# Performance work log

Measured on AMD Instinct MI355X. Metric: run time of the kernel, lower is better.

Reference implementation:

```python
import jax, jax.numpy as jnp
import numpy as np

NUM_HEADS = 16
HEAD_DIM = 128
HIDDEN = NUM_HEADS * HEAD_DIM


def rotate_half(x):
    x1, x2 = jnp.split(x, 2, axis=-1)
    return jnp.concatenate((-x2, x1), axis=-1)


def setup_inputs() -> dict:
    key = jax.random.key(0)
    ks = jax.random.split(key, 7)
    b, s = 2, 2048
    return {
        "hidden_states": jax.random.normal(ks[0], (b, s, HIDDEN), dtype=jnp.float32),
        "cos": jax.random.normal(ks[1], (1, 1, s, HEAD_DIM), dtype=jnp.float32),
        "sin": jax.random.normal(ks[2], (1, 1, s, HEAD_DIM), dtype=jnp.float32),
        "Wq": jax.random.normal(ks[3], (HIDDEN, HIDDEN), dtype=jnp.float32) * 0.02,
        "Wk": jax.random.normal(ks[4], (HIDDEN, HIDDEN), dtype=jnp.float32) * 0.02,
        "Wv": jax.random.normal(ks[5], (HIDDEN, HIDDEN), dtype=jnp.float32) * 0.02,
        "Wo": jax.random.normal(ks[6], (HIDDEN, HIDDEN), dtype=jnp.float32) * 0.02,
    }


def reference(hidden_states, cos, sin, Wq, Wk, Wv, Wo):
    b, s, _ = hidden_states.shape

    def proj(W):
        # [b,s,hidden] -> [b,H,s,D]
        return (hidden_states @ W).reshape(b, s, NUM_HEADS, HEAD_DIM).transpose(0, 2, 1, 3)

    q = proj(Wq)
    k = proj(Wk)
    v = proj(Wv)

    # RoPE: cos/sin [1,1,s,D] broadcast over batch and heads
    q = q * cos + rotate_half(q) * sin
    k = k * cos + rotate_half(k) * sin

    scale = 1.0 / jnp.sqrt(jnp.asarray(HEAD_DIM, dtype=q.dtype))
    scores = jnp.einsum("bhqd,bhkd->bhqk", q, k) * scale  # [b,H,s,s]
    attn = jax.nn.softmax(scores, axis=-1)  # no mask applied (matches source)
    out = jnp.einsum("bhqk,bhkd->bhqd", attn, v)  # [b,H,s,D]
    out = out.transpose(0, 2, 1, 3).reshape(b, s, HIDDEN)
    return out @ Wo
```

## Files before the change

kernel.cpp:

```cpp
#include <hip/hip_runtime.h>

typedef short bf16x8 __attribute__((ext_vector_type(8)));
typedef float f32x4 __attribute__((ext_vector_type(4)));

#define HID   2048
#define S_LEN 2048
#define NH    16
#define HD    128
#define BATCH 2
#define NROWS (BATCH * S_LEN)

__device__ __forceinline__ float bf2f(unsigned short u) {
    union { unsigned int i; float f; } v;
    v.i = ((unsigned int)u) << 16;
    return v.f;
}
__device__ __forceinline__ unsigned short f2bf(float f) {
    union { float f; unsigned int i; } v;
    v.f = f;
    unsigned int u = v.i;
    return (unsigned short)((u + 0x7fffu + ((u >> 16) & 1u)) >> 16);
}

__device__ __forceinline__ void async16(const unsigned short* g, unsigned short* l) {
    __builtin_amdgcn_global_load_lds(
        (const __attribute__((address_space(1))) unsigned int*)g,
        (__attribute__((address_space(3))) unsigned int*)l, 16, 0, 0);
}

__global__ __launch_bounds__(256) void cast_f32_bf16(const float* __restrict__ x,
                                                     unsigned short* __restrict__ y, int n) {
    int i = (blockIdx.x * 256 + threadIdx.x) * 4;
    if (i < n) {
        float4 v = *(const float4*)(x + i);
        ushort4 o;
        o.x = f2bf(v.x); o.y = f2bf(v.y); o.z = f2bf(v.z); o.w = f2bf(v.w);
        *(ushort4*)(y + i) = o;
    }
}

__global__ __launch_bounds__(256) void transpose_cast(const float* __restrict__ W,
                                                      unsigned short* __restrict__ WT) {
    __shared__ float tile[32][33];
    int tx = threadIdx.x, ty = threadIdx.y;
    int bx = blockIdx.x, by = blockIdx.y;
#pragma unroll
    for (int i = 0; i < 4; i++)
        tile[ty + i * 8][tx] = W[(size_t)(by * 32 + ty + i * 8) * HID + bx * 32 + tx];
    __syncthreads();
#pragma unroll
    for (int i = 0; i < 4; i++)
        WT[(size_t)(bx * 32 + ty + i * 8) * HID + by * 32 + tx] = f2bf(tile[tx][ty + i * 8]);
}

template <int MODE>
__global__ __launch_bounds__(256, 2) void gemm_bt(const unsigned short* __restrict__ A,
                                                  const unsigned short* __restrict__ Bt,
                                                  void* __restrict__ Cout) {
    __shared__ unsigned short Asm[128 * 32];
    __shared__ unsigned short Bsm[128 * 32];
    int t = threadIdx.x;
    int wave = t >> 6, lane = t & 63;
    int wm = wave >> 1, wn = wave & 1;
    int c = lane & 15, quad = lane >> 4;
    int m0 = blockIdx.y * 128, n0 = blockIdx.x * 128;

    int srow = wave * 32 + (lane >> 2);
    int scol = (lane & 3) * 8;
    const unsigned short* Ag = A + (size_t)(m0 + srow) * HID + scol;
    const unsigned short* Bg = Bt + (size_t)(n0 + srow) * HID + scol;
    unsigned short* Al = Asm + wave * 1024;
    unsigned short* Bl = Bsm + wave * 1024;

    f32x4 zero = {0.f, 0.f, 0.f, 0.f};
    f32x4 acc[4][4];
#pragma unroll
    for (int i = 0; i < 4; i++)
#pragma unroll
        for (int j = 0; j < 4; j++) acc[i][j] = zero;

    for (int k0 = 0; k0 < HID; k0 += 32) {
        async16(Ag + k0, Al);
        async16(Ag + k0 + 16 * HID, Al + 512);
        async16(Bg + k0, Bl);
        async16(Bg + k0 + 16 * HID, Bl + 512);
        __syncthreads();
        bf16x8 af[4], bfr[4];
#pragma unroll
        for (int mt = 0; mt < 4; mt++)
            af[mt] = *(const bf16x8*)(Asm + (wm * 64 + mt * 16 + c) * 32 + quad * 8);
#pragma unroll
        for (int nt = 0; nt < 4; nt++)
            bfr[nt] = *(const bf16x8*)(Bsm + (wn * 64 + nt * 16 + c) * 32 + quad * 8);
#pragma unroll
        for (int mt = 0; mt < 4; mt++)
#pragma unroll
            for (int nt = 0; nt < 4; nt++)
                acc[mt][nt] = __builtin_amdgcn_mfma_f32_16x16x32_bf16(af[mt], bfr[nt],
                                                                      acc[mt][nt], 0, 0, 0);
        __syncthreads();
    }

#pragma unroll
    for (int mt = 0; mt < 4; mt++) {
#pragma unroll
        for (int nt = 0; nt < 4; nt++) {
#pragma unroll
            for (int r = 0; r < 4; r++) {
                int row = m0 + wm * 64 + mt * 16 + quad * 4 + r;
                int col = n0 + wn * 64 + nt * 16 + c;
                float v = acc[mt][nt][r];
                if (MODE == 2) {
                    ((float*)Cout)[(size_t)row * HID + col] = v;
                } else {
                    int b = row >> 11, s = row & 2047;
                    int h = col >> 7, d = col & 127;
                    size_t idx;
                    if (MODE == 0) idx = ((size_t)(b * NH + h) * S_LEN + s) * HD + d;
                    else           idx = ((size_t)(b * NH + h) * HD + d) * S_LEN + s;
                    ((unsigned short*)Cout)[idx] = f2bf(v);
                }
            }
        }
    }
}

__global__ __launch_bounds__(256) void rope_kernel(unsigned short* __restrict__ Qb,
                                                   unsigned short* __restrict__ Kb,
                                                   const float* __restrict__ cosp,
                                                   const float* __restrict__ sinp) {
    unsigned short* P = blockIdx.y ? Kb : Qb;
    float scq = blockIdx.y ? 1.0f : 0.08838834764831845f;
    int idx = blockIdx.x * 256 + threadIdx.x;
    int row = idx >> 6, j = idx & 63;
    int s = row & (S_LEN - 1);
    size_t base = (size_t)row * HD;
    float x1 = bf2f(P[base + j]);
    float x2 = bf2f(P[base + j + 64]);
    float c1 = cosp[s * HD + j], s1 = sinp[s * HD + j];
    float c2 = cosp[s * HD + j + 64], s2 = sinp[s * HD + j + 64];
    P[base + j]      = f2bf((x1 * c1 - x2 * s1) * scq);
    P[base + j + 64] = f2bf((x2 * c2 + x1 * s2) * scq);
}

#define PKS 72
__global__ __launch_bounds__(256, 2) void attn_kernel(const unsigned short* __restrict__ Q,
                                                      const unsigned short* __restrict__ Kg,
                                                      const unsigned short* __restrict__ Vt,
                                                      unsigned short* __restrict__ Aout) {
    __shared__ unsigned short Ksm[64 * 128];
    __shared__ unsigned short Vsm[128 * 64];
    __shared__ __align__(16) unsigned short Psm[4 * 2 * 16 * PKS];
    int bh = blockIdx.y;
    int b = bh >> 4, h = bh & 15;
    int t = threadIdx.x;
    int wave = t >> 6, lane = t & 63;
    int c = lane & 15, quad = lane >> 4;
    int q0 = blockIdx.x * 128 + wave * 32;
    const unsigned short* Qp = Q + (size_t)bh * S_LEN * HD;
    const unsigned short* Kp = Kg + (size_t)bh * S_LEN * HD;
    const unsigned short* Vp = Vt + (size_t)bh * HD * S_LEN;

    bf16x8 qf[2][4];
#pragma unroll
    for (int qn = 0; qn < 2; qn++)
#pragma unroll
        for (int kk = 0; kk < 4; kk++)
            qf[qn][kk] = *(const bf16x8*)(Qp + (size_t)(q0 + qn * 16 + c) * HD + kk * 32 + quad * 8);

    f32x4 zero = {0.f, 0.f, 0.f, 0.f};
    f32x4 o_acc[2][8];
#pragma unroll
    for (int qn = 0; qn < 2; qn++)
#pragma unroll
        for (int nt = 0; nt < 8; nt++) o_acc[qn][nt] = zero;
    float lsum[2] = {0.f, 0.f};

    for (int key0 = 0; key0 < S_LEN; key0 += 64) {
#pragma unroll
        for (int j = 0; j < 4; j++) {
            int fc = (wave * 4 + j) * 64 + lane;
            int rK = fc >> 4, cbK = (fc & 15) ^ (rK & 15);
            async16(Kp + (size_t)(key0 + rK) * HD + cbK * 8, Ksm + (wave * 4 + j) * 512);
            int rV = fc >> 3, cbV = (fc & 7) ^ (rV & 7);
            async16(Vp + (size_t)rV * S_LEN + key0 + cbV * 8, Vsm + (wave * 4 + j) * 512);
        }
        __syncthreads();

        f32x4 sacc[4][2];
#pragma unroll
        for (int km = 0; km < 4; km++)
#pragma unroll
            for (int qn = 0; qn < 2; qn++) sacc[km][qn] = zero;
#pragma unroll
        for (int kk = 0; kk < 4; kk++) {
            bf16x8 kfr[4];
#pragma unroll
            for (int km = 0; km < 4; km++)
                kfr[km] = *(const bf16x8*)(Ksm + (km * 16 + c) * HD + (((kk * 4 + quad) ^ c)) * 8);
#pragma unroll
            for (int km = 0; km < 4; km++)
#pragma unroll
                for (int qn = 0; qn < 2; qn++)
                    sacc[km][qn] = __builtin_amdgcn_mfma_f32_16x16x32_bf16(kfr[km], qf[qn][kk],
                                                                           sacc[km][qn], 0, 0, 0);
        }

#pragma unroll
        for (int qn = 0; qn < 2; qn++) {
#pragma unroll
            for (int km = 0; km < 4; km++) {
                float e0 = __expf(sacc[km][qn][0]);
                float e1 = __expf(sacc[km][qn][1]);
                float e2 = __expf(sacc[km][qn][2]);
                float e3 = __expf(sacc[km][qn][3]);
                lsum[qn] += (e0 + e1) + (e2 + e3);
                uint2 pk;
                pk.x = (unsigned int)f2bf(e0) | ((unsigned int)f2bf(e1) << 16);
                pk.y = (unsigned int)f2bf(e2) | ((unsigned int)f2bf(e3) << 16);
                *(uint2*)(Psm + ((wave * 2 + qn) * 16 + c) * PKS + km * 16 + quad * 4) = pk;
            }
        }
        asm volatile("" ::: "memory");
        __builtin_amdgcn_s_waitcnt(0xc07f);
        asm volatile("" ::: "memory");

#pragma unroll
        for (int kf = 0; kf < 2; kf++) {
            bf16x8 pf[2];
#pragma unroll
            for (int qn = 0; qn < 2; qn++)
                pf[qn] = *(const bf16x8*)(Psm + ((wave * 2 + qn) * 16 + c) * PKS + kf * 32 + quad * 8);
#pragma unroll
            for (int nt = 0; nt < 8; nt++) {
                bf16x8 vf = *(const bf16x8*)(Vsm + (nt * 16 + c) * 64 +
                                             (((kf * 4 + quad) ^ (c & 7))) * 8);
#pragma unroll
                for (int qn = 0; qn < 2; qn++)
                    o_acc[qn][nt] = __builtin_amdgcn_mfma_f32_16x16x32_bf16(pf[qn], vf,
                                                                            o_acc[qn][nt], 0, 0, 0);
            }
        }
        __syncthreads();
    }

#pragma unroll
    for (int qn = 0; qn < 2; qn++) {
        lsum[qn] += __shfl_xor(lsum[qn], 16);
        lsum[qn] += __shfl_xor(lsum[qn], 32);
    }
    float inv[2][4];
#pragma unroll
    for (int qn = 0; qn < 2; qn++)
#pragma unroll
        for (int r = 0; r < 4; r++)
            inv[qn][r] = 1.0f / __shfl(lsum[qn], quad * 4 + r);

#pragma unroll
    for (int qn = 0; qn < 2; qn++) {
#pragma unroll
        for (int r = 0; r < 4; r++) {
            int srow = q0 + qn * 16 + quad * 4 + r;
            size_t base = ((size_t)(b * S_LEN + srow)) * HID + h * HD;
#pragma unroll
            for (int nt = 0; nt < 8; nt++)
                Aout[base + nt * 16 + c] = f2bf(o_acc[qn][nt][r] * inv[qn][r]);
        }
    }
}

extern "C" void kernel_launch(void* const* d_in, const int* in_sizes, int n_in,
                              void* d_out, int out_size, void* d_ws, size_t ws_size,
                              hipStream_t stream) {
    const float* hs   = (const float*)d_in[0];
    const float* cosp = (const float*)d_in[1];
    const float* sinp = (const float*)d_in[2];
    const float* Wq   = (const float*)d_in[3];
    const float* Wk   = (const float*)d_in[4];
    const float* Wv   = (const float*)d_in[5];
    const float* Wo   = (const float*)d_in[6];

    char* ws = (char*)d_ws;
    unsigned short* Xb = (unsigned short*)(ws);
    unsigned short* WT = (unsigned short*)(ws + (16ull << 20));
    unsigned short* Qb = (unsigned short*)(ws + (24ull << 20));
    unsigned short* Kb = (unsigned short*)(ws + (40ull << 20));
    unsigned short* Vb = (unsigned short*)(ws + (56ull << 20));

    dim3 tb(32, 8);
    dim3 tg(64, 64);
    dim3 gg(16, 32);

    cast_f32_bf16<<<8192, 256, 0, stream>>>(hs, Xb, NROWS * HID);

    transpose_cast<<<tg, tb, 0, stream>>>(Wq, WT);
    gemm_bt<0><<<gg, 256, 0, stream>>>(Xb, WT, Qb);

    transpose_cast<<<tg, tb, 0, stream>>>(Wk, WT);
    gemm_bt<0><<<gg, 256, 0, stream>>>(Xb, WT, Kb);

    transpose_cast<<<tg, tb, 0, stream>>>(Wv, WT);
    gemm_bt<1><<<gg, 256, 0, stream>>>(Xb, WT, Vb);

    rope_kernel<<<dim3(16384, 2), 256, 0, stream>>>(Qb, Kb, cosp, sinp);

    attn_kernel<<<dim3(16, 32), 256, 0, stream>>>(Qb, Kb, Vb, Xb );

    transpose_cast<<<tg, tb, 0, stream>>>(Wo, WT);
    gemm_bt<2><<<gg, 256, 0, stream>>>(Xb, WT, d_out);
}
```

Baseline: 448.6 us.

## Fuse QKV projections into one GEMM launch and use exp2/packed bf16 conversion

```diff
diff --git a/kernel.cpp b/kernel.cpp
--- a/kernel.cpp
+++ b/kernel.cpp
@@ -22,6 +22,26 @@
     return (unsigned short)((u + 0x7fffu + ((u >> 16) & 1u)) >> 16);
 }
 
+__device__ __forceinline__ unsigned int pkbf(float a, float b) {
+#if defined(__has_builtin) && __has_builtin(__builtin_amdgcn_cvt_pk_bf16_f32)
+    typedef __bf16 bf2_t __attribute__((ext_vector_type(2)));
+    bf2_t v = __builtin_amdgcn_cvt_pk_bf16_f32(a, b);
+    unsigned int u;
+    __builtin_memcpy(&u, &v, 4);
+    return u;
+#else
+    return (unsigned int)f2bf(a) | ((unsigned int)f2bf(b) << 16);
+#endif
+}
+
+__device__ __forceinline__ float exp2_fast(float x) {
+#if defined(__has_builtin) && __has_builtin(__builtin_amdgcn_exp2f)
+    return __builtin_amdgcn_exp2f(x);
+#else
+    return __expf(x * 0.6931471805599453f);
+#endif
+}
+
 __device__ __forceinline__ void async16(const unsigned short* g, unsigned short* l) {
     __builtin_amdgcn_global_load_lds(
         (const __attribute__((address_space(1))) unsigned int*)g,
@@ -33,42 +53,51 @@
     int i = (blockIdx.x * 256 + threadIdx.x) * 4;
     if (i < n) {
         float4 v = *(const float4*)(x + i);
-        ushort4 o;
-        o.x = f2bf(v.x); o.y = f2bf(v.y); o.z = f2bf(v.z); o.w = f2bf(v.w);
-        *(ushort4*)(y + i) = o;
-    }
-}
-
-__global__ __launch_bounds__(256) void transpose_cast(const float* __restrict__ W,
+        uint2 o;
+        o.x = pkbf(v.x, v.y);
+        o.y = pkbf(v.z, v.w);
+        *(uint2*)(y + i) = o;
+    }
+}
+
+__global__ __launch_bounds__(256) void transpose_cast(const float* __restrict__ Wa,
+                                                      const float* __restrict__ Wb,
+                                                      const float* __restrict__ Wc,
                                                       unsigned short* __restrict__ WT) {
     __shared__ float tile[32][33];
     int tx = threadIdx.x, ty = threadIdx.y;
-    int bx = blockIdx.x, by = blockIdx.y;
+    int bx = blockIdx.x, by = blockIdx.y, z = blockIdx.z;
+    const float* W = (z == 0) ? Wa : ((z == 1) ? Wb : Wc);
+    unsigned short* dst = WT + (size_t)z * HID * HID;
 #pragma unroll
     for (int i = 0; i < 4; i++)
         tile[ty + i * 8][tx] = W[(size_t)(by * 32 + ty + i * 8) * HID + bx * 32 + tx];
     __syncthreads();
 #pragma unroll
     for (int i = 0; i < 4; i++)
-        WT[(size_t)(bx * 32 + ty + i * 8) * HID + by * 32 + tx] = f2bf(tile[tx][ty + i * 8]);
+        dst[(size_t)(bx * 32 + ty + i * 8) * HID + by * 32 + tx] = f2bf(tile[tx][ty + i * 8]);
 }
 
 template <int MODE>
-__global__ __launch_bounds__(256, 2) void gemm_bt(const unsigned short* __restrict__ A,
+__global__ __launch_bounds__(256, 3) void gemm_bt(const unsigned short* __restrict__ A,
                                                   const unsigned short* __restrict__ Bt,
-                                                  void* __restrict__ Cout) {
+                                                  unsigned short* __restrict__ Qo,
+                                                  unsigned short* __restrict__ Ko,
+                                                  unsigned short* __restrict__ Vo,
+                                                  float* __restrict__ Fo,
+                                                  int n_shift) {
     __shared__ unsigned short Asm[128 * 32];
     __shared__ unsigned short Bsm[128 * 32];
     int t = threadIdx.x;
     int wave = t >> 6, lane = t & 63;
     int wm = wave >> 1, wn = wave & 1;
     int c = lane & 15, quad = lane >> 4;
-    int m0 = blockIdx.y * 128, n0 = blockIdx.x * 128;
+    int m0 = blockIdx.y * 128, nloc = blockIdx.x * 128;
 
     int srow = wave * 32 + (lane >> 2);
     int scol = (lane & 3) * 8;
     const unsigned short* Ag = A + (size_t)(m0 + srow) * HID + scol;
-    const unsigned short* Bg = Bt + (size_t)(n0 + srow) * HID + scol;
+    const unsigned short* Bg = Bt + (size_t)(nloc + srow) * HID + scol;
     unsigned short* Al = Asm + wave * 1024;
     unsigned short* Bl = Bsm + wave * 1024;
 
@@ -101,24 +130,44 @@
         __syncthreads();
     }
 
-#pragma unroll
-    for (int mt = 0; mt < 4; mt++) {
-#pragma unroll
-        for (int nt = 0; nt < 4; nt++) {
-#pragma unroll
-            for (int r = 0; r < 4; r++) {
-                int row = m0 + wm * 64 + mt * 16 + quad * 4 + r;
-                int col = n0 + wn * 64 + nt * 16 + c;
-                float v = acc[mt][nt][r];
-                if (MODE == 2) {
-                    ((float*)Cout)[(size_t)row * HID + col] = v;
+    if (MODE == 2) {
+#pragma unroll
+        for (int mt = 0; mt < 4; mt++)
+#pragma unroll
+            for (int nt = 0; nt < 4; nt++)
+#pragma unroll
+                for (int r = 0; r < 4; r++) {
+                    int row = m0 + wm * 64 + mt * 16 + quad * 4 + r;
+                    int col = nloc + wn * 64 + nt * 16 + c;
+                    Fo[(size_t)row * HID + col] = acc[mt][nt][r];
+                }
+    } else {
+        int nglob0 = n_shift + nloc;
+        int mat = nglob0 >> 11;
+        int ncol0 = nglob0 & 2047;
+        unsigned short* Cb = (mat == 0) ? Qo : ((mat == 1) ? Ko : Vo);
+#pragma unroll
+        for (int mt = 0; mt < 4; mt++) {
+#pragma unroll
+            for (int nt = 0; nt < 4; nt++) {
+                int colm = ncol0 + wn * 64 + nt * 16 + c;
+                int h = colm >> 7, d = colm & 127;
+                if (mat < 2) {
+#pragma unroll
+                    for (int r = 0; r < 4; r++) {
+                        int row = m0 + wm * 64 + mt * 16 + quad * 4 + r;
+                        int b = row >> 11, s = row & 2047;
+                        Cb[((size_t)(b * NH + h) * S_LEN + s) * HD + d] = f2bf(acc[mt][nt][r]);
+                    }
                 } else {
-                    int b = row >> 11, s = row & 2047;
-                    int h = col >> 7, d = col & 127;
-                    size_t idx;
-                    if (MODE == 0) idx = ((size_t)(b * NH + h) * S_LEN + s) * HD + d;
-                    else           idx = ((size_t)(b * NH + h) * HD + d) * S_LEN + s;
-                    ((unsigned short*)Cout)[idx] = f2bf(v);
+                    int row0 = m0 + wm * 64 + mt * 16 + quad * 4;
+                    int b = row0 >> 11, s = row0 & 2047;
+                    ushort4 o;
+                    o.x = f2bf(acc[mt][nt][0]);
+                    o.y = f2bf(acc[mt][nt][1]);
+                    o.z = f2bf(acc[mt][nt][2]);
+                    o.w = f2bf(acc[mt][nt][3]);
+                    *(ushort4*)(Cb + ((size_t)(b * NH + h) * HD + d) * S_LEN + s) = o;
                 }
             }
         }
@@ -130,7 +179,7 @@
                                                    const float* __restrict__ cosp,
                                                    const float* __restrict__ sinp) {
     unsigned short* P = blockIdx.y ? Kb : Qb;
-    float scq = blockIdx.y ? 1.0f : 0.08838834764831845f;
+    float scq = blockIdx.y ? 1.0f : 0.12751743f;
     int idx = blockIdx.x * 256 + threadIdx.x;
     int row = idx >> 6, j = idx & 63;
     int s = row & (S_LEN - 1);
@@ -210,14 +259,14 @@
         for (int qn = 0; qn < 2; qn++) {
 #pragma unroll
             for (int km = 0; km < 4; km++) {
-                float e0 = __expf(sacc[km][qn][0]);
-                float e1 = __expf(sacc[km][qn][1]);
-                float e2 = __expf(sacc[km][qn][2]);
-                float e3 = __expf(sacc[km][qn][3]);
+                float e0 = exp2_fast(sacc[km][qn][0]);
+                float e1 = exp2_fast(sacc[km][qn][1]);
+                float e2 = exp2_fast(sacc[km][qn][2]);
+                float e3 = exp2_fast(sacc[km][qn][3]);
                 lsum[qn] += (e0 + e1) + (e2 + e3);
                 uint2 pk;
-                pk.x = (unsigned int)f2bf(e0) | ((unsigned int)f2bf(e1) << 16);
-                pk.y = (unsigned int)f2bf(e2) | ((unsigned int)f2bf(e3) << 16);
+                pk.x = pkbf(e0, e1);
+                pk.y = pkbf(e2, e3);
                 *(uint2*)(Psm + ((wave * 2 + qn) * 16 + c) * PKS + km * 16 + quad * 4) = pk;
             }
         }
@@ -282,30 +331,34 @@
 
     char* ws = (char*)d_ws;
     unsigned short* Xb = (unsigned short*)(ws);
-    unsigned short* WT = (unsigned short*)(ws + (16ull << 20));
-    unsigned short* Qb = (unsigned short*)(ws + (24ull << 20));
-    unsigned short* Kb = (unsigned short*)(ws + (40ull << 20));
-    unsigned short* Vb = (unsigned short*)(ws + (56ull << 20));
+    unsigned short* Qb = (unsigned short*)(ws + (16ull << 20));
+    unsigned short* Kb = (unsigned short*)(ws + (32ull << 20));
+    unsigned short* Vb = (unsigned short*)(ws + (48ull << 20));
+    unsigned short* WT = (unsigned short*)(ws + (64ull << 20));
+
+    const bool fused = ws_size >= (88ull << 20);
 
     dim3 tb(32, 8);
-    dim3 tg(64, 64);
-    dim3 gg(16, 32);
 
     cast_f32_bf16<<<8192, 256, 0, stream>>>(hs, Xb, NROWS * HID);
 
-    transpose_cast<<<tg, tb, 0, stream>>>(Wq, WT);
-    gemm_bt<0><<<gg, 256, 0, stream>>>(Xb, WT, Qb);
-
-    transpose_cast<<<tg, tb, 0, stream>>>(Wk, WT);
-    gemm_bt<0><<<gg, 256, 0, stream>>>(Xb, WT, Kb);
-
-    transpose_cast<<<tg, tb, 0, stream>>>(Wv, WT);
-    gemm_bt<1><<<gg, 256, 0, stream>>>(Xb, WT, Vb);
+    if (fused) {
+        transpose_cast<<<dim3(64, 64, 3), tb, 0, stream>>>(Wq, Wk, Wv, WT);
+        gemm_bt<0><<<dim3(48, 32), 256, 0, stream>>>(Xb, WT, Qb, Kb, Vb, nullptr, 0);
+    } else {
+        transpose_cast<<<dim3(64, 64, 1), tb, 0, stream>>>(Wq, Wq, Wq, WT);
+        gemm_bt<0><<<dim3(16, 32), 256, 0, stream>>>(Xb, WT, Qb, Kb, Vb, nullptr, 0);
+        transpose_cast<<<dim3(64, 64, 1), tb, 0, stream>>>(Wk, Wk, Wk, WT);
+        gemm_bt<0><<<dim3(16, 32), 256, 0, stream>>>(Xb, WT, Qb, Kb, Vb, nullptr, 2048);
+        transpose_cast<<<dim3(64, 64, 1), tb, 0, stream>>>(Wv, Wv, Wv, WT);
+        gemm_bt<0><<<dim3(16, 32), 256, 0, stream>>>(Xb, WT, Qb, Kb, Vb, nullptr, 4096);
+    }
 
     rope_kernel<<<dim3(16384, 2), 256, 0, stream>>>(Qb, Kb, cosp, sinp);
 
     attn_kernel<<<dim3(16, 32), 256, 0, stream>>>(Qb, Kb, Vb, Xb );
 
-    transpose_cast<<<tg, tb, 0, stream>>>(Wo, WT);
-    gemm_bt<2><<<gg, 256, 0, stream>>>(Xb, WT, d_out);
-}
+    transpose_cast<<<dim3(64, 64, 1), tb, 0, stream>>>(Wo, Wo, Wo, WT);
+    gemm_bt<2><<<dim3(16, 32), 256, 0, stream>>>(Xb, WT, nullptr, nullptr, nullptr,
+                                                 (float*)d_out, 0);
+}
```

Measured after the change: 422.7 us. 1.06x faster.
